# Optimization experiments

Hardware: AMD Instinct MI355X
Metric: run time of the kernel (lower is better)

## Reference

```python
import jax, jax.numpy as jnp
import numpy as np

B, N, DIM, H, DH = 2, 2048, 1024, 16, 64
INNER = H * DH


def _rotate_half(t):
    # interleaved pairs: (..., d) -> rotate each (x1, x2) pair to (-x2, x1)
    t = t.reshape(*t.shape[:-1], -1, 2)
    x1, x2 = t[..., 0], t[..., 1]
    return jnp.stack((-x2, x1), axis=-1).reshape(*t.shape[:-2], -1)


def _apply_rotary(freqs, t):
    # freqs: [B, N, DH] -> broadcast over heads; t: [B, H, N, DH]
    f = freqs[:, None, :, :]
    return t * jnp.cos(f) + _rotate_half(t) * jnp.sin(f)


def _layernorm(x, g, b, eps=1e-5):
    mu = jnp.mean(x, axis=-1, keepdims=True)
    var = jnp.mean((x - mu) ** 2, axis=-1, keepdims=True)
    return (x - mu) * jax.lax.rsqrt(var + eps) * g + b


def setup_inputs() -> dict:
    key = jax.random.key(0)
    ks = jax.random.split(key, 8)
    x = jax.random.normal(ks[0], (B, N, DIM), jnp.float32)
    rotary = jax.random.normal(ks[1], (B, N, DH), jnp.float32)
    ln_g = jnp.ones((DIM,), jnp.float32)
    ln_b = jnp.zeros((DIM,), jnp.float32)
    w_qkv = jax.random.normal(ks[2], (DIM, 3 * INNER), jnp.float32) / np.sqrt(DIM)
    b_qkv = jnp.zeros((3 * INNER,), jnp.float32)
    w_out = jax.random.normal(ks[3], (INNER, DIM), jnp.float32) / np.sqrt(INNER)
    b_out = jnp.zeros((DIM,), jnp.float32)
    return {"x": x, "rotary": rotary, "ln_g": ln_g, "ln_b": ln_b,
            "w_qkv": w_qkv, "b_qkv": b_qkv, "w_out": w_out, "b_out": b_out}


def reference(x, rotary, ln_g, ln_b, w_qkv, b_qkv, w_out, b_out):
    h = _layernorm(x, ln_g, ln_b)
    qkv = h @ w_qkv + b_qkv                      # [B, N, 3*INNER]
    q, k, v = jnp.split(qkv, 3, axis=-1)
    # b n (h d) -> b h n d
    def to_heads(t):
        return t.reshape(B, N, H, DH).transpose(0, 2, 1, 3)
    q, k, v = to_heads(q), to_heads(k), to_heads(v)
    q = _apply_rotary(rotary, q)
    k = _apply_rotary(rotary, k)
    v = _apply_rotary(rotary, v)                 # rotate_value=True
    scale = DH ** (-0.5)
    attn = jnp.einsum('bhnd,bhmd->bhnm', q, k) * scale
    attn = jax.nn.softmax(attn, axis=-1)
    out = jnp.einsum('bhnm,bhmd->bhnd', attn, v)
    out = _apply_rotary(-rotary, out)            # inverse rotation on values
    out = out.transpose(0, 2, 1, 3).reshape(B, N, INNER)
    return out @ w_out + b_out
```

## Files before the change

kernel.cpp:

```cpp
#include <hip/hip_runtime.h>
#include <hip/hip_bf16.h>

typedef _Float16 f16;
typedef __attribute__((ext_vector_type(4))) float f32x4;
typedef __attribute__((ext_vector_type(8))) _Float16 f16x8;
typedef __attribute__((ext_vector_type(4))) _Float16 f16x4;
typedef __attribute__((ext_vector_type(2))) __fp16 hf2;

#define Bv 2
#define Nv 2048
#define DIMv 1024
#define Hv 16
#define DHv 64
#define INNERv 1024
#define QKV3v 3072

__device__ __forceinline__ void gload16(const void* g, void* l) {
  __builtin_amdgcn_global_load_lds(
      (const __attribute__((address_space(1))) void*)g,
      (__attribute__((address_space(3))) void*)l, 16, 0, 0);
}

__global__ __launch_bounds__(256) void ln_kernel(
    const float* __restrict__ x, const float* __restrict__ g,
    const float* __restrict__ bb, f16* __restrict__ h) {
  const int row = blockIdx.x;
  const int t = threadIdx.x;
  const float4 v = reinterpret_cast<const float4*>(x + (size_t)row * DIMv)[t];
  float s = v.x + v.y + v.z + v.w;
  float sq = v.x * v.x + v.y * v.y + v.z * v.z + v.w * v.w;
#pragma unroll
  for (int o = 32; o > 0; o >>= 1) {
    s += __shfl_down(s, o);
    sq += __shfl_down(sq, o);
  }
  __shared__ float red[8];
  __shared__ float musr[2];
  const int wave = t >> 6, lane = t & 63;
  if (lane == 0) { red[wave] = s; red[4 + wave] = sq; }
  __syncthreads();
  if (t == 0) {
    const float S = red[0] + red[1] + red[2] + red[3];
    const float SQ = red[4] + red[5] + red[6] + red[7];
    const float mu = S * (1.0f / DIMv);
    const float var = SQ * (1.0f / DIMv) - mu * mu;
    musr[0] = mu;
    musr[1] = rsqrtf(var + 1e-5f);
  }
  __syncthreads();
  const float mu = musr[0], rs = musr[1];
  const float4 gv = reinterpret_cast<const float4*>(g)[t];
  const float4 bv = reinterpret_cast<const float4*>(bb)[t];
  f16x4 o;
  o.x = (f16)((v.x - mu) * rs * gv.x + bv.x);
  o.y = (f16)((v.y - mu) * rs * gv.y + bv.y);
  o.z = (f16)((v.z - mu) * rs * gv.z + bv.z);
  o.w = (f16)((v.w - mu) * rs * gv.w + bv.w);
  *reinterpret_cast<f16x4*>(&h[(size_t)row * DIMv + t * 4]) = o;
}

__global__ __launch_bounds__(256) void rotcs_kernel(
    const float* __restrict__ rot, float* __restrict__ c,
    float* __restrict__ s, int n) {
  const int i = blockIdx.x * blockDim.x + threadIdx.x;
  if (i < n) {
    const float f = rot[i];
    c[i] = cosf(f);
    s[i] = sinf(f);
  }
}

__global__ __launch_bounds__(256) void transpose_f16(
    const float* __restrict__ W, f16* __restrict__ Wt, int K, int N) {
  __shared__ float tile[64][65];
  const int t = threadIdx.x;
  const int n0 = blockIdx.x * 64, k0 = blockIdx.y * 64;
#pragma unroll
  for (int i = 0; i < 16; ++i) {
    const int idx = t + i * 256;
    const int r = idx >> 6, c = idx & 63;
    tile[r][c] = W[(size_t)(k0 + r) * N + n0 + c];
  }
  __syncthreads();
#pragma unroll
  for (int i = 0; i < 16; ++i) {
    const int idx = t + i * 256;
    const int r = idx >> 6, c = idx & 63;
    Wt[(size_t)(n0 + r) * K + k0 + c] = (f16)tile[c][r];
  }
}

template <int EPI>
__global__ __launch_bounds__(256) void gemm_mfma(
    const f16* __restrict__ A, const f16* __restrict__ Bt,
    const float* __restrict__ bias, void* __restrict__ Cout,
    const float* __restrict__ cs, const float* __restrict__ sn,
    int M, int N, int K) {
  __shared__ __align__(16) f16 Asb[2][128 * 32];
  __shared__ __align__(16) f16 Bsb[2][128 * 32];
  const int t = threadIdx.x;
  const int l = t & 63, w = t >> 6;
  const int wr = w >> 1, wc = w & 1;
  const int row0 = blockIdx.y * 128, col0 = blockIdx.x * 128;

  const int i1 = t, i2 = t + 256;
  const f16* ga1 = &A[(size_t)(row0 + (i1 >> 2)) * K + (i1 & 3) * 8];
  const f16* ga2 = &A[(size_t)(row0 + (i2 >> 2)) * K + (i2 & 3) * 8];
  const f16* gb1 = &Bt[(size_t)(col0 + (i1 >> 2)) * K + (i1 & 3) * 8];
  const f16* gb2 = &Bt[(size_t)(col0 + (i2 >> 2)) * K + (i2 & 3) * 8];
  const int a_off1 = w * 512, a_off2 = w * 512 + 2048;

  const int rl = l & 15, kg = l >> 4;
  const int ar = (wr * 64 + rl) * 32 + kg * 8;
  const int br = (wc * 64 + rl) * 32 + kg * 8;

  const f32x4 zero = {0.f, 0.f, 0.f, 0.f};
  f32x4 acc[4][4];
#pragma unroll
  for (int m = 0; m < 4; ++m)
#pragma unroll
    for (int n = 0; n < 4; ++n) acc[m][n] = zero;

#define GSTAGE(buf, kk)                           \
  {                                               \
    gload16(ga1 + (kk)*32, &Asb[buf][a_off1]);    \
    gload16(ga2 + (kk)*32, &Asb[buf][a_off2]);    \
    gload16(gb1 + (kk)*32, &Bsb[buf][a_off1]);    \
    gload16(gb2 + (kk)*32, &Bsb[buf][a_off2]);    \
  }

  const int nt = K >> 5;
  GSTAGE(0, 0);

  for (int kt = 0; kt < nt; ++kt) {
    const int cur = kt & 1;
    if (kt + 1 < nt) {
      GSTAGE(cur ^ 1, kt + 1);
      asm volatile("s_waitcnt vmcnt(4)" ::: "memory");
    } else {
      asm volatile("s_waitcnt vmcnt(0)" ::: "memory");
    }
    __builtin_amdgcn_s_barrier();
    __builtin_amdgcn_sched_barrier(0);
    f16x8 af[4], bf[4];
#pragma unroll
    for (int m = 0; m < 4; ++m)
      af[m] = *reinterpret_cast<const f16x8*>(&Asb[cur][ar + m * 16 * 32]);
#pragma unroll
    for (int n = 0; n < 4; ++n)
      bf[n] = *reinterpret_cast<const f16x8*>(&Bsb[cur][br + n * 16 * 32]);
#pragma unroll
    for (int m = 0; m < 4; ++m)
#pragma unroll
      for (int n = 0; n < 4; ++n)
        acc[m][n] =
            __builtin_amdgcn_mfma_f32_16x16x32_f16(af[m], bf[n], acc[m][n], 0, 0, 0);
    asm volatile("" ::: "memory");
    __builtin_amdgcn_s_barrier();
    __builtin_amdgcn_sched_barrier(0);
  }
#undef GSTAGE

#pragma unroll
  for (int m = 0; m < 4; ++m) {
#pragma unroll
    for (int n = 0; n < 4; ++n) {
#pragma unroll
      for (int jr = 0; jr < 4; ++jr) {
        const int rg = row0 + wr * 64 + m * 16 + kg * 4 + jr;
        const int cg = col0 + wc * 64 + n * 16 + rl;
        const float v = acc[m][n][jr] + bias[cg];
        if (EPI == 0) {
          ((float*)Cout)[(size_t)rg * N + cg] = v;
        } else {
          const float p = __shfl_xor(v, 1);
          const size_t cb = (size_t)rg * DHv + (cg & 63);
          const float cc = cs[cb], ss = sn[cb];
          const float y = (l & 1) ? (v * cc + p * ss) : (v * cc - p * ss);
          ((f16*)Cout)[(size_t)rg * N + cg] = (f16)y;
        }
      }
    }
  }
}

__global__ __launch_bounds__(256) void prep_kv(
    const f16* __restrict__ qkvf, f16* __restrict__ Kimg,
    f16* __restrict__ Vimg) {
  const int nt = blockIdx.x, hh = blockIdx.y, b = blockIdx.z;
  const int t = threadIdx.x;
  const size_t tbase = ((size_t)((b * Hv + hh) * 32 + nt)) << 12;

#pragma unroll
  for (int half = 0; half < 2; ++half) {
    const int task = t + half * 256;
    const int key = task >> 3, c = task & 7;
    const int d = (c * 8) ^ ((key & 7) << 3);
    const f16x8 kv = *reinterpret_cast<const f16x8*>(
        &qkvf[(size_t)(b * Nv + nt * 64 + key) * QKV3v + INNERv + hh * DHv + d]);
    *reinterpret_cast<f16x8*>(&Kimg[tbase + key * 64 + c * 8]) = kv;
  }

  __shared__ __align__(16) f16 tile[64][80];
  const int nl = t >> 3, dc = (t & 7) * 8;
#pragma unroll
  for (int half = 0; half < 2; ++half) {
    const int n = nl + half * 32;
    *reinterpret_cast<f16x8*>(&tile[n][dc]) = *reinterpret_cast<const f16x8*>(
        &qkvf[(size_t)(b * Nv + nt * 64 + n) * QKV3v + 2 * INNERv + hh * DHv + dc]);
  }
  __syncthreads();
  const int c0 = (t & 7) * 8;
  const int kwp = c0 >> 5, kgp = (c0 >> 3) & 3;
#pragma unroll
  for (int half = 0; half < 2; ++half) {
    const int d = (t >> 3) + half * 32;
    union { f16 e[8]; f16x8 v; } uo;
#pragma unroll
    for (int j = 0; j < 8; ++j) {
      const int mk = (j >> 2) & 1, jr = j & 3;
      const int kap = kwp * 32 + mk * 16 + kgp * 4 + jr;
      uo.e[j] = tile[kap][d];
    }
    *reinterpret_cast<f16x8*>(
        &Vimg[tbase + d * 64 + (c0 ^ ((d & 7) << 3))]) = uo.v;
  }
}

__global__ __launch_bounds__(512, 4) void attn_mfma(
    const f16* __restrict__ qkvf, const f16* __restrict__ Kimg,
    const f16* __restrict__ Vimg, const float* __restrict__ cs,
    const float* __restrict__ sn, f16* __restrict__ ao) {
  const int wg = blockIdx.x;
  const int swz = (wg & 7) * 64 + (wg >> 3);
  const int qb = swz & 15;
  const int hh = (swz >> 4) & 15;
  const int b = swz >> 8;
  const int t = threadIdx.x, l = t & 63, w = t >> 6;
  const int qw = w >> 1, kw = w & 1;
  const int rl = l & 15, kg = l >> 4;

  __shared__ __align__(16) f16 KsB[2][4096];
  __shared__ __align__(16) f16 VtB[2][4096];
  __shared__ float Lbuf[4][2][32];

  const size_t qrow0 = (size_t)(b * Nv + qb * 128 + qw * 32);
  f16x8 bq[2][2];
#pragma unroll
  for (int nq = 0; nq < 2; ++nq)
#pragma unroll
    for (int ks = 0; ks < 2; ++ks)
      bq[nq][ks] = *reinterpret_cast<const f16x8*>(
          &qkvf[(qrow0 + nq * 16 + rl) * QKV3v + hh * DHv + ks * 32 + kg * 8]);

  f16x8 ones;
#pragma unroll
  for (int j = 0; j < 8; ++j) ones[j] = (f16)1.0f;

  const f32x4 zero = {0.f, 0.f, 0.f, 0.f};
  f32x4 o_acc[2][4];
  f32x4 l_acc[2] = {zero, zero};
#pragma unroll
  for (int nq = 0; nq < 2; ++nq)
#pragma unroll
    for (int m2 = 0; m2 < 4; ++m2) o_acc[nq][m2] = zero;

  const size_t ibase = (((size_t)((b * Hv + hh) * 32)) << 12) + w * 512 + l * 8;
  const f16* kimg_t = Kimg + ibase;
  const f16* vimg_t = Vimg + ibase;

#define STAGEI(buf, tile)                                   \
  {                                                         \
    gload16(kimg_t + ((size_t)(tile) << 12), &KsB[buf][w * 512]); \
    gload16(vimg_t + ((size_t)(tile) << 12), &VtB[buf][w * 512]); \
  }

  STAGEI(0, 0);

  const float SC2 = 0.125f * 1.44269504f;

  for (int kt = 0; kt < 32; ++kt) {
    const int cur = kt & 1;
    if (kt + 1 < 32) {
      STAGEI(cur ^ 1, kt + 1);
      asm volatile("s_waitcnt vmcnt(2)" ::: "memory");
    } else {
      asm volatile("s_waitcnt vmcnt(0)" ::: "memory");
    }
    __builtin_amdgcn_s_barrier();
    __builtin_amdgcn_sched_barrier(0);

    const f16* Kc = &KsB[cur][0];
    const f16* Vc = &VtB[cur][0];

    f16x8 ak[2][2];
#pragma unroll
    for (int mk = 0; mk < 2; ++mk)
#pragma unroll
      for (int ks = 0; ks < 2; ++ks)
        ak[mk][ks] = *reinterpret_cast<const f16x8*>(
            &Kc[((kw * 32 + mk * 16 + rl) << 6) |
                ((ks * 32 + kg * 8) ^ ((rl & 7) << 3))]);
    f16x8 av[4];
#pragma unroll
    for (int m2 = 0; m2 < 4; ++m2)
      av[m2] = *reinterpret_cast<const f16x8*>(
          &Vc[((m2 * 16 + rl) << 6) |
              ((kw * 32 + kg * 8) ^ ((rl & 7) << 3))]);

    f32x4 sa[2][2];
#pragma unroll
    for (int mk = 0; mk < 2; ++mk)
#pragma unroll
      for (int nq = 0; nq < 2; ++nq) sa[mk][nq] = zero;
    __builtin_amdgcn_s_setprio(1);
#pragma unroll
    for (int ks = 0; ks < 2; ++ks)
#pragma unroll
      for (int mk = 0; mk < 2; ++mk)
#pragma unroll
        for (int nq = 0; nq < 2; ++nq)
          sa[mk][nq] = __builtin_amdgcn_mfma_f32_16x16x32_f16(
              ak[mk][ks], bq[nq][ks], sa[mk][nq], 0, 0, 0);
    __builtin_amdgcn_s_setprio(0);

    f16x8 pb[2];
#pragma unroll
    for (int nq = 0; nq < 2; ++nq) {
      float p00 = exp2f(fminf(sa[0][nq][0] * SC2, 13.0f));
      float p01 = exp2f(fminf(sa[0][nq][1] * SC2, 13.0f));
      float p02 = exp2f(fminf(sa[0][nq][2] * SC2, 13.0f));
      float p03 = exp2f(fminf(sa[0][nq][3] * SC2, 13.0f));
      float p10 = exp2f(fminf(sa[1][nq][0] * SC2, 13.0f));
      float p11 = exp2f(fminf(sa[1][nq][1] * SC2, 13.0f));
      float p12 = exp2f(fminf(sa[1][nq][2] * SC2, 13.0f));
      float p13 = exp2f(fminf(sa[1][nq][3] * SC2, 13.0f));
      union { hf2 h2[4]; f16x8 v; } u;
      u.h2[0] = __builtin_amdgcn_cvt_pkrtz(p00, p01);
      u.h2[1] = __builtin_amdgcn_cvt_pkrtz(p02, p03);
      u.h2[2] = __builtin_amdgcn_cvt_pkrtz(p10, p11);
      u.h2[3] = __builtin_amdgcn_cvt_pkrtz(p12, p13);
      pb[nq] = u.v;
    }

    __builtin_amdgcn_s_setprio(1);
#pragma unroll
    for (int nq = 0; nq < 2; ++nq)
      l_acc[nq] = __builtin_amdgcn_mfma_f32_16x16x32_f16(
          ones, pb[nq], l_acc[nq], 0, 0, 0);
#pragma unroll
    for (int nq = 0; nq < 2; ++nq)
#pragma unroll
      for (int m2 = 0; m2 < 4; ++m2)
        o_acc[nq][m2] = __builtin_amdgcn_mfma_f32_16x16x32_f16(
            av[m2], pb[nq], o_acc[nq][m2], 0, 0, 0);
    __builtin_amdgcn_s_setprio(0);

    asm volatile("" ::: "memory");
    __builtin_amdgcn_s_barrier();
    __builtin_amdgcn_sched_barrier(0);
  }
#undef STAGEI

  if (kg == 0) {
    Lbuf[qw][kw][rl] = l_acc[0][0];
    Lbuf[qw][kw][16 + rl] = l_acc[1][0];
  }
  char* ob = (qw < 2 ? (char*)KsB : (char*)VtB) + (qw & 1) * 8192;
  if (kw == 1) {
#pragma unroll
    for (int nq = 0; nq < 2; ++nq)
#pragma unroll
      for (int m2 = 0; m2 < 4; ++m2)
        *reinterpret_cast<f32x4*>(
            ob + (nq * 16 + rl) * 256 +
            ((m2 * 64 + kg * 16) ^ ((rl & 7) << 4))) = o_acc[nq][m2];
  }
  __syncthreads();
  if (kw == 0) {
#pragma unroll
    for (int nq = 0; nq < 2; ++nq)
#pragma unroll
      for (int m2 = 0; m2 < 4; ++m2) {
        f32x4* slot = reinterpret_cast<f32x4*>(
            ob + (nq * 16 + rl) * 256 +
            ((m2 * 64 + kg * 16) ^ ((rl & 7) << 4)));
        *slot = *slot + o_acc[nq][m2];
      }
  }
  __syncthreads();
  {
    const int q_local = w * 16 + (l >> 2);
    const int qw_r = q_local >> 5, q_in = q_local & 31;
    const int d0 = (l & 3) * 16;
    char* rb = (qw_r < 2 ? (char*)KsB : (char*)VtB) + (qw_r & 1) * 8192;
    const float linv = 1.0f / (Lbuf[qw_r][0][q_in] + Lbuf[qw_r][1][q_in]);
    const size_t nq_g = (size_t)(b * Nv + qb * 128 + q_local);
    const size_t cb = nq_g * DHv + d0;
    union { f16 e[16]; f16x8 v[2]; } uo;
#pragma unroll
    for (int j = 0; j < 4; ++j) {
      const unsigned off = q_in * 256 + (((l & 3) * 64 + j * 16) ^ ((q_in & 7) << 4));
      const f32x4 a = *reinterpret_cast<const f32x4*>(rb + off);
      const float4 csv = *reinterpret_cast<const float4*>(&cs[cb + j * 4]);
      const float4 snv = *reinterpret_cast<const float4*>(&sn[cb + j * 4]);
      const float o0 = a[0] * linv;
      const float o1 = a[1] * linv;
      const float o2 = a[2] * linv;
      const float o3 = a[3] * linv;
      uo.e[j * 4 + 0] = (f16)(o0 * csv.x + o1 * snv.x);
      uo.e[j * 4 + 1] = (f16)(o1 * csv.y - o0 * snv.y);
      uo.e[j * 4 + 2] = (f16)(o2 * csv.z + o3 * snv.z);
      uo.e[j * 4 + 3] = (f16)(o3 * csv.w - o2 * snv.w);
    }
    f16* aop = &ao[nq_g * INNERv + hh * DHv + d0];
    *reinterpret_cast<f16x8*>(aop) = uo.v[0];
    *reinterpret_cast<f16x8*>(aop + 8) = uo.v[1];
  }
}

extern "C" void kernel_launch(void* const* d_in, const int* in_sizes, int n_in,
                              void* d_out, int out_size, void* d_ws, size_t ws_size,
                              hipStream_t stream) {
  (void)in_sizes; (void)n_in; (void)out_size; (void)ws_size;
  const float* x = (const float*)d_in[0];
  const float* rot = (const float*)d_in[1];
  const float* ln_g = (const float*)d_in[2];
  const float* ln_b = (const float*)d_in[3];
  const float* w_qkv = (const float*)d_in[4];
  const float* b_qkv = (const float*)d_in[5];
  const float* w_out = (const float*)d_in[6];
  const float* b_out = (const float*)d_in[7];

  char* p = (char*)d_ws;
  f16* h = (f16*)p;            p += (size_t)Bv * Nv * DIMv * 2;
  float* cs = (float*)p;       p += (size_t)Bv * Nv * DHv * 4;
  float* sn = (float*)p;       p += (size_t)Bv * Nv * DHv * 4;
  f16* wqT = (f16*)p;          p += (size_t)QKV3v * DIMv * 2;
  f16* woT = (f16*)p;          p += (size_t)DIMv * INNERv * 2;
  f16* qkvf = (f16*)p;         p += (size_t)Bv * Nv * QKV3v * 2;
  f16* ao = (f16*)p;           p += (size_t)Bv * Nv * INNERv * 2;
  f16* Kimg = (f16*)p;         p += (size_t)Bv * Hv * 32 * 4096 * 2;
  f16* Vimg = (f16*)p;         p += (size_t)Bv * Hv * 32 * 4096 * 2;

  ln_kernel<<<dim3(Bv * Nv), dim3(256), 0, stream>>>(x, ln_g, ln_b, h);
  rotcs_kernel<<<dim3((Bv * Nv * DHv) / 256), dim3(256), 0, stream>>>(
      rot, cs, sn, Bv * Nv * DHv);
  transpose_f16<<<dim3(QKV3v / 64, DIMv / 64), dim3(256), 0, stream>>>(
      w_qkv, wqT, DIMv, QKV3v);
  transpose_f16<<<dim3(INNERv / 64, DIMv / 64), dim3(256), 0, stream>>>(
      w_out, woT, DIMv, INNERv);
  gemm_mfma<1><<<dim3(QKV3v / 128, (Bv * Nv) / 128), dim3(256), 0, stream>>>(
      h, wqT, b_qkv, (void*)qkvf, cs, sn, Bv * Nv, QKV3v, DIMv);
  prep_kv<<<dim3(Nv / 64, Hv, Bv), dim3(256), 0, stream>>>(qkvf, Kimg, Vimg);
  attn_mfma<<<dim3(512), dim3(512), 0, stream>>>(qkvf, Kimg, Vimg, cs, sn, ao);
  gemm_mfma<0><<<dim3(DIMv / 128, (Bv * Nv) / 128), dim3(256), 0, stream>>>(
      ao, woT, b_out, d_out, nullptr, nullptr, Bv * Nv, DIMv, INNERv);
}
```

Measured before the change: 160.8 us.

## Fuse QKV GEMM with K/V tile-image scatter using 256x256 MFMA tiles

Replaces the 128x128 QKV GEMM and the separate prep_kv kernel with one 256x256-tile, 512-thread GEMM. It uses a BK=64 swizzled LDS double buffer with direct global-to-LDS loads. The epilogue applies rotary and writes Q row-major, while K and V go straight into the swizzled tile images the attention kernel expects. This removes a kernel launch and a full read/write pass over K and V. The cost is larger tiles: only 12x16 = 192 blocks, which can underfill the GPU, plus heavier register and LDS pressure and scattered 2-byte K stores.

```diff
diff --git a/kernel.cpp b/kernel.cpp
--- a/kernel.cpp
+++ b/kernel.cpp
@@ -87,6 +87,129 @@
     const int idx = t + i * 256;
     const int r = idx >> 6, c = idx & 63;
     Wt[(size_t)(n0 + r) * K + k0 + c] = (f16)tile[c][r];
+  }
+}
+
+__global__ __launch_bounds__(512) void gemm256_qkv(
+    const f16* __restrict__ A, const f16* __restrict__ Bt,
+    const float* __restrict__ bias, f16* __restrict__ qkvf,
+    f16* __restrict__ Kimg, f16* __restrict__ Vimg,
+    const float* __restrict__ cs, const float* __restrict__ sn) {
+  __shared__ __align__(16) f16 Abuf[2][256 * 64];
+  __shared__ __align__(16) f16 Bbuf[2][256 * 64];
+  const int t = threadIdx.x, l = t & 63, w = t >> 6;
+  const int wm = w >> 2, wn = w & 3;
+  const int row0 = blockIdx.y * 256, col0 = blockIdx.x * 256;
+  const int rl = l & 15, kg = l >> 4;
+
+  const int srow = l >> 3;
+  const int sgk = ((l & 7) ^ (srow & 7)) * 8;
+  const f16* gA = &A[(size_t)(row0 + w * 32 + srow) * 1024 + sgk];
+  const f16* gB = &Bt[(size_t)(col0 + w * 32 + srow) * 1024 + sgk];
+
+  const f32x4 zero = {0.f, 0.f, 0.f, 0.f};
+  f32x4 acc[8][4];
+#pragma unroll
+  for (int m = 0; m < 8; ++m)
+#pragma unroll
+    for (int n = 0; n < 4; ++n) acc[m][n] = zero;
+
+#define STG(buf, kt)                                                         \
+  {                                                                          \
+    _Pragma("unroll") for (int i = 0; i < 4; ++i)                            \
+        gload16(gA + (kt)*64 + i * 8 * 1024,                                 \
+                &Abuf[buf][(w * 32 + i * 8) * 64]);                          \
+    _Pragma("unroll") for (int i = 0; i < 4; ++i)                            \
+        gload16(gB + (kt)*64 + i * 8 * 1024,                                 \
+                &Bbuf[buf][(w * 32 + i * 8) * 64]);                          \
+  }
+
+  const int nkt = 16;
+  STG(0, 0);
+
+  for (int kt = 0; kt < nkt; ++kt) {
+    const int cur = kt & 1;
+    if (kt + 1 < nkt) {
+      STG(cur ^ 1, kt + 1);
+      asm volatile("s_waitcnt vmcnt(8)" ::: "memory");
+    } else {
+      asm volatile("s_waitcnt vmcnt(0)" ::: "memory");
+    }
+    __builtin_amdgcn_s_barrier();
+    __builtin_amdgcn_sched_barrier(0);
+#pragma unroll
+    for (int kh = 0; kh < 2; ++kh) {
+      f16x8 bf[4], af[8];
+#pragma unroll
+      for (int n = 0; n < 4; ++n) {
+        const int r = wn * 64 + n * 16 + rl;
+        bf[n] = *reinterpret_cast<const f16x8*>(
+            &Bbuf[cur][r * 64 + (((kh * 4 + kg) ^ (r & 7)) << 3)]);
+      }
+#pragma unroll
+      for (int m = 0; m < 8; ++m) {
+        const int r = wm * 128 + m * 16 + rl;
+        af[m] = *reinterpret_cast<const f16x8*>(
+            &Abuf[cur][r * 64 + (((kh * 4 + kg) ^ (r & 7)) << 3)]);
+      }
+      __builtin_amdgcn_s_setprio(1);
+#pragma unroll
+      for (int m = 0; m < 8; ++m)
+#pragma unroll
+        for (int n = 0; n < 4; ++n)
+          acc[m][n] = __builtin_amdgcn_mfma_f32_16x16x32_f16(af[m], bf[n],
+                                                             acc[m][n], 0, 0, 0);
+      __builtin_amdgcn_s_setprio(0);
+    }
+    asm volatile("" ::: "memory");
+    __builtin_amdgcn_s_barrier();
+    __builtin_amdgcn_sched_barrier(0);
+  }
+#undef STG
+
+  const int slab = col0 >> 10;
+  const int b = row0 >> 11;
+#pragma unroll
+  for (int m = 0; m < 8; ++m) {
+    const int rg = row0 + wm * 128 + m * 16 + kg * 4;
+    const int nt = (rg & 2047) >> 6;
+#pragma unroll
+    for (int n = 0; n < 4; ++n) {
+      const int cg = col0 + wn * 64 + n * 16 + rl;
+      const int d = cg & 63;
+      const int hh = (cg >> 6) & 15;
+      float y[4];
+#pragma unroll
+      for (int jr = 0; jr < 4; ++jr) {
+        const float v = acc[m][n][jr] + bias[cg];
+        const float p = __shfl_xor(v, 1);
+        const size_t cb = (size_t)(rg + jr) * DHv + d;
+        const float cc = cs[cb], ss = sn[cb];
+        y[jr] = (l & 1) ? (v * cc + p * ss) : (v * cc - p * ss);
+      }
+      if (slab == 0) {
+#pragma unroll
+        for (int jr = 0; jr < 4; ++jr)
+          qkvf[(size_t)(rg + jr) * QKV3v + cg] = (f16)y[jr];
+      } else if (slab == 1) {
+        const size_t tb = ((size_t)((b * Hv + hh) * 32 + nt)) << 12;
+#pragma unroll
+        for (int jr = 0; jr < 4; ++jr) {
+          const int key = ((m & 3) * 16 + kg * 4 + jr);
+          Kimg[tb + key * 64 + (d ^ ((key & 7) << 3))] = (f16)y[jr];
+        }
+      } else {
+        const size_t tb = ((size_t)((b * Hv + hh) * 32 + nt)) << 12;
+        const int kp = ((m & 2) << 4) | (kg << 3);
+        f16x4 pk;
+        pk.x = (f16)y[0];
+        pk.y = (f16)y[1];
+        pk.z = (f16)y[2];
+        pk.w = (f16)y[3];
+        *reinterpret_cast<f16x4*>(
+            &Vimg[tb + d * 64 + (kp ^ ((d & 7) << 3)) + ((m & 1) << 2)]) = pk;
+      }
+    }
   }
 }
 
@@ -181,49 +304,6 @@
         }
       }
     }
-  }
-}
-
-__global__ __launch_bounds__(256) void prep_kv(
-    const f16* __restrict__ qkvf, f16* __restrict__ Kimg,
-    f16* __restrict__ Vimg) {
-  const int nt = blockIdx.x, hh = blockIdx.y, b = blockIdx.z;
-  const int t = threadIdx.x;
-  const size_t tbase = ((size_t)((b * Hv + hh) * 32 + nt)) << 12;
-
-#pragma unroll
-  for (int half = 0; half < 2; ++half) {
-    const int task = t + half * 256;
-    const int key = task >> 3, c = task & 7;
-    const int d = (c * 8) ^ ((key & 7) << 3);
-    const f16x8 kv = *reinterpret_cast<const f16x8*>(
-        &qkvf[(size_t)(b * Nv + nt * 64 + key) * QKV3v + INNERv + hh * DHv + d]);
-    *reinterpret_cast<f16x8*>(&Kimg[tbase + key * 64 + c * 8]) = kv;
-  }
-
-  __shared__ __align__(16) f16 tile[64][80];
-  const int nl = t >> 3, dc = (t & 7) * 8;
-#pragma unroll
-  for (int half = 0; half < 2; ++half) {
-    const int n = nl + half * 32;
-    *reinterpret_cast<f16x8*>(&tile[n][dc]) = *reinterpret_cast<const f16x8*>(
-        &qkvf[(size_t)(b * Nv + nt * 64 + n) * QKV3v + 2 * INNERv + hh * DHv + dc]);
-  }
-  __syncthreads();
-  const int c0 = (t & 7) * 8;
-  const int kwp = c0 >> 5, kgp = (c0 >> 3) & 3;
-#pragma unroll
-  for (int half = 0; half < 2; ++half) {
-    const int d = (t >> 3) + half * 32;
-    union { f16 e[8]; f16x8 v; } uo;
-#pragma unroll
-    for (int j = 0; j < 8; ++j) {
-      const int mk = (j >> 2) & 1, jr = j & 3;
-      const int kap = kwp * 32 + mk * 16 + kgp * 4 + jr;
-      uo.e[j] = tile[kap][d];
-    }
-    *reinterpret_cast<f16x8*>(
-        &Vimg[tbase + d * 64 + (c0 ^ ((d & 7) << 3))]) = uo.v;
   }
 }
 
@@ -450,9 +530,8 @@
       w_qkv, wqT, DIMv, QKV3v);
   transpose_f16<<<dim3(INNERv / 64, DIMv / 64), dim3(256), 0, stream>>>(
       w_out, woT, DIMv, INNERv);
-  gemm_mfma<1><<<dim3(QKV3v / 128, (Bv * Nv) / 128), dim3(256), 0, stream>>>(
-      h, wqT, b_qkv, (void*)qkvf, cs, sn, Bv * Nv, QKV3v, DIMv);
-  prep_kv<<<dim3(Nv / 64, Hv, Bv), dim3(256), 0, stream>>>(qkvf, Kimg, Vimg);
+  gemm256_qkv<<<dim3(QKV3v / 256, (Bv * Nv) / 256), dim3(512), 0, stream>>>(
+      h, wqT, b_qkv, qkvf, Kimg, Vimg, cs, sn);
   attn_mfma<<<dim3(512), dim3(512), 0, stream>>>(qkvf, Kimg, Vimg, cs, sn, ao);
   gemm_mfma<0><<<dim3(DIMv / 128, (Bv * Nv) / 128), dim3(256), 0, stream>>>(
       ao, woT, b_out, d_out, nullptr, nullptr, Bv * Nv, DIMv, INNERv);
```

After: 151.3 us. 5.9% less time.

## Fuse K/V image packing into QKV GEMM epilogue; triple-buffer attention K/V tiles

Applied to the files above, without the earlier changes.

The QKV GEMM epilogue now writes rotated Q to qkvf and scatters rotated K and V straight into the swizzled tile images used by attention. This removes the separate prep_kv kernel and its extra read and write of K/V. The attention loop also moves from double to triple buffering of K/V tiles in LDS with a prefetch distance of two. The cost is more LDS per block, which may reduce occupancy, and scattered 2-byte K stores from the GEMM epilogue.

```diff
diff --git a/kernel.cpp b/kernel.cpp
--- a/kernel.cpp
+++ b/kernel.cpp
@@ -95,6 +95,7 @@
     const f16* __restrict__ A, const f16* __restrict__ Bt,
     const float* __restrict__ bias, void* __restrict__ Cout,
     const float* __restrict__ cs, const float* __restrict__ sn,
+    f16* __restrict__ qkvf, f16* __restrict__ Kimg, f16* __restrict__ Vimg,
     int M, int N, int K) {
   __shared__ __align__(16) f16 Asb[2][128 * 32];
   __shared__ __align__(16) f16 Bsb[2][128 * 32];
@@ -161,69 +162,65 @@
   }
 #undef GSTAGE
 
-#pragma unroll
-  for (int m = 0; m < 4; ++m) {
-#pragma unroll
-    for (int n = 0; n < 4; ++n) {
-#pragma unroll
-      for (int jr = 0; jr < 4; ++jr) {
-        const int rg = row0 + wr * 64 + m * 16 + kg * 4 + jr;
-        const int cg = col0 + wc * 64 + n * 16 + rl;
-        const float v = acc[m][n][jr] + bias[cg];
-        if (EPI == 0) {
-          ((float*)Cout)[(size_t)rg * N + cg] = v;
-        } else {
-          const float p = __shfl_xor(v, 1);
-          const size_t cb = (size_t)rg * DHv + (cg & 63);
-          const float cc = cs[cb], ss = sn[cb];
-          const float y = (l & 1) ? (v * cc + p * ss) : (v * cc - p * ss);
-          ((f16*)Cout)[(size_t)rg * N + cg] = (f16)y;
+  if (EPI == 0) {
+#pragma unroll
+    for (int m = 0; m < 4; ++m) {
+#pragma unroll
+      for (int n = 0; n < 4; ++n) {
+#pragma unroll
+        for (int jr = 0; jr < 4; ++jr) {
+          const int rg = row0 + wr * 64 + m * 16 + kg * 4 + jr;
+          const int cg = col0 + wc * 64 + n * 16 + rl;
+          ((float*)Cout)[(size_t)rg * N + cg] = acc[m][n][jr] + bias[cg];
         }
       }
     }
-  }
-}
-
-__global__ __launch_bounds__(256) void prep_kv(
-    const f16* __restrict__ qkvf, f16* __restrict__ Kimg,
-    f16* __restrict__ Vimg) {
-  const int nt = blockIdx.x, hh = blockIdx.y, b = blockIdx.z;
-  const int t = threadIdx.x;
-  const size_t tbase = ((size_t)((b * Hv + hh) * 32 + nt)) << 12;
-
-#pragma unroll
-  for (int half = 0; half < 2; ++half) {
-    const int task = t + half * 256;
-    const int key = task >> 3, c = task & 7;
-    const int d = (c * 8) ^ ((key & 7) << 3);
-    const f16x8 kv = *reinterpret_cast<const f16x8*>(
-        &qkvf[(size_t)(b * Nv + nt * 64 + key) * QKV3v + INNERv + hh * DHv + d]);
-    *reinterpret_cast<f16x8*>(&Kimg[tbase + key * 64 + c * 8]) = kv;
-  }
-
-  __shared__ __align__(16) f16 tile[64][80];
-  const int nl = t >> 3, dc = (t & 7) * 8;
-#pragma unroll
-  for (int half = 0; half < 2; ++half) {
-    const int n = nl + half * 32;
-    *reinterpret_cast<f16x8*>(&tile[n][dc]) = *reinterpret_cast<const f16x8*>(
-        &qkvf[(size_t)(b * Nv + nt * 64 + n) * QKV3v + 2 * INNERv + hh * DHv + dc]);
-  }
-  __syncthreads();
-  const int c0 = (t & 7) * 8;
-  const int kwp = c0 >> 5, kgp = (c0 >> 3) & 3;
-#pragma unroll
-  for (int half = 0; half < 2; ++half) {
-    const int d = (t >> 3) + half * 32;
-    union { f16 e[8]; f16x8 v; } uo;
-#pragma unroll
-    for (int j = 0; j < 8; ++j) {
-      const int mk = (j >> 2) & 1, jr = j & 3;
-      const int kap = kwp * 32 + mk * 16 + kgp * 4 + jr;
-      uo.e[j] = tile[kap][d];
-    }
-    *reinterpret_cast<f16x8*>(
-        &Vimg[tbase + d * 64 + (c0 ^ ((d & 7) << 3))]) = uo.v;
+  } else {
+    const int slab = col0 >> 10;
+    const int b = row0 >> 11;
+    const int ntile = ((row0 & 2047) >> 6) + wr;
+#pragma unroll
+    for (int m = 0; m < 4; ++m) {
+      const int key0 = m * 16 + kg * 4;
+      const int rgb = row0 + wr * 64 + key0;
+#pragma unroll
+      for (int n = 0; n < 4; ++n) {
+        const int cg = col0 + wc * 64 + n * 16 + rl;
+        const int d = cg & 63;
+        const int hh = (cg >> 6) & 15;
+        float y[4];
+#pragma unroll
+        for (int jr = 0; jr < 4; ++jr) {
+          const float v = acc[m][n][jr] + bias[cg];
+          const float p = __shfl_xor(v, 1);
+          const size_t cb = (size_t)(rgb + jr) * DHv + d;
+          const float cc = cs[cb], ss = sn[cb];
+          y[jr] = (l & 1) ? (v * cc + p * ss) : (v * cc - p * ss);
+        }
+        if (slab == 0) {
+#pragma unroll
+          for (int jr = 0; jr < 4; ++jr)
+            qkvf[(size_t)(rgb + jr) * QKV3v + cg] = (f16)y[jr];
+        } else if (slab == 1) {
+          const size_t tb = ((size_t)((b * Hv + hh) * 32 + ntile)) << 12;
+#pragma unroll
+          for (int jr = 0; jr < 4; ++jr) {
+            const int key = key0 + jr;
+            Kimg[tb + key * 64 + (d ^ ((key & 7) << 3))] = (f16)y[jr];
+          }
+        } else {
+          const size_t tb = ((size_t)((b * Hv + hh) * 32 + ntile)) << 12;
+          const int kp = ((m & 2) << 4) | (kg << 3);
+          f16x4 pk;
+          pk.x = (f16)y[0];
+          pk.y = (f16)y[1];
+          pk.z = (f16)y[2];
+          pk.w = (f16)y[3];
+          *reinterpret_cast<f16x4*>(
+              &Vimg[tb + d * 64 + (kp ^ ((d & 7) << 3)) + ((m & 1) << 2)]) = pk;
+        }
+      }
+    }
   }
 }
 
@@ -240,8 +237,8 @@
   const int qw = w >> 1, kw = w & 1;
   const int rl = l & 15, kg = l >> 4;
 
-  __shared__ __align__(16) f16 KsB[2][4096];
-  __shared__ __align__(16) f16 VtB[2][4096];
+  __shared__ __align__(16) f16 KsB[3][4096];
+  __shared__ __align__(16) f16 VtB[3][4096];
   __shared__ float Lbuf[4][2][32];
 
   const size_t qrow0 = (size_t)(b * Nv + qb * 128 + qw * 32);
@@ -269,20 +266,25 @@
   const f16* kimg_t = Kimg + ibase;
   const f16* vimg_t = Vimg + ibase;
 
-#define STAGEI(buf, tile)                                   \
-  {                                                         \
+#define STAGEI(buf, tile)                                         \
+  {                                                               \
     gload16(kimg_t + ((size_t)(tile) << 12), &KsB[buf][w * 512]); \
     gload16(vimg_t + ((size_t)(tile) << 12), &VtB[buf][w * 512]); \
   }
 
   STAGEI(0, 0);
+  STAGEI(1, 1);
 
   const float SC2 = 0.125f * 1.44269504f;
 
+  int cur = 0;
   for (int kt = 0; kt < 32; ++kt) {
-    const int cur = kt & 1;
-    if (kt + 1 < 32) {
-      STAGEI(cur ^ 1, kt + 1);
+    if (kt < 30) {
+      int stg = cur + 2;
+      if (stg >= 3) stg -= 3;
+      STAGEI(stg, kt + 2);
+      asm volatile("s_waitcnt vmcnt(4)" ::: "memory");
+    } else if (kt == 30) {
       asm volatile("s_waitcnt vmcnt(2)" ::: "memory");
     } else {
       asm volatile("s_waitcnt vmcnt(0)" ::: "memory");
@@ -359,6 +361,7 @@
     asm volatile("" ::: "memory");
     __builtin_amdgcn_s_barrier();
     __builtin_amdgcn_sched_barrier(0);
+    cur = (cur == 2) ? 0 : cur + 1;
   }
 #undef STAGEI
 
@@ -450,10 +453,10 @@
       w_qkv, wqT, DIMv, QKV3v);
   transpose_f16<<<dim3(INNERv / 64, DIMv / 64), dim3(256), 0, stream>>>(
       w_out, woT, DIMv, INNERv);
-  gemm_mfma<1><<<dim3(QKV3v / 128, (Bv * Nv) / 128), dim3(256), 0, stream>>>(
-      h, wqT, b_qkv, (void*)qkvf, cs, sn, Bv * Nv, QKV3v, DIMv);
-  prep_kv<<<dim3(Nv / 64, Hv, Bv), dim3(256), 0, stream>>>(qkvf, Kimg, Vimg);
+  gemm_mfma<2><<<dim3(QKV3v / 128, (Bv * Nv) / 128), dim3(256), 0, stream>>>(
+      h, wqT, b_qkv, nullptr, cs, sn, qkvf, Kimg, Vimg, Bv * Nv, QKV3v, DIMv);
   attn_mfma<<<dim3(512), dim3(512), 0, stream>>>(qkvf, Kimg, Vimg, cs, sn, ao);
   gemm_mfma<0><<<dim3(DIMv / 128, (Bv * Nv) / 128), dim3(256), 0, stream>>>(
-      ao, woT, b_out, d_out, nullptr, nullptr, Bv * Nv, DIMv, INNERv);
-}
+      ao, woT, b_out, d_out, nullptr, nullptr, nullptr, nullptr, nullptr,
+      Bv * Nv, DIMv, INNERv);
+}
```

Result: no change. 159.6 us (-0.8%).
